# Optimization experiments

Measured on AMD Instinct MI355X. Metric: run time of the kernel, lower is better.

## Reference

```python
import jax, jax.numpy as jnp
import numpy as np
import math

B, T, D = 8, 1024, 1024
N, L = 256, 768
H = 16
TE = 2048  # time_embed_dim
EPS = 1e-5


def _ln(x, g, b):
    mu = jnp.mean(x, axis=-1, keepdims=True)
    var = jnp.mean(jnp.square(x - mu), axis=-1, keepdims=True)
    return (x - mu) * jax.lax.rsqrt(var + EPS) * g + b


def setup_inputs() -> dict:
    key = jax.random.key(0)
    ks = jax.random.split(key, 16)
    s = lambda fan_in: 1.0 / math.sqrt(fan_in)
    return {
        "x": jax.random.normal(ks[0], (B, T, D), jnp.float32),
        "xf": jax.random.normal(ks[1], (B, N, L), jnp.float32),
        "emb": jax.random.normal(ks[2], (B, TE), jnp.float32),
        "ln_g": jnp.ones((D,), jnp.float32),
        "ln_b": jnp.zeros((D,), jnp.float32),
        "cln_g": jnp.ones((L,), jnp.float32),
        "cln_b": jnp.zeros((L,), jnp.float32),
        "Wq": jax.random.normal(ks[3], (D, D), jnp.float32) * s(D),
        "bq": jnp.zeros((D,), jnp.float32),
        "Wk": jax.random.normal(ks[4], (L, D), jnp.float32) * s(L),
        "bk": jnp.zeros((D,), jnp.float32),
        "Wv": jax.random.normal(ks[5], (L, D), jnp.float32) * s(L),
        "bv": jnp.zeros((D,), jnp.float32),
        "sln_g": jnp.ones((D,), jnp.float32),
        "sln_b": jnp.zeros((D,), jnp.float32),
        "Wemb": jax.random.normal(ks[6], (TE, 2 * D), jnp.float32) * s(TE),
        "bemb": jnp.zeros((2 * D,), jnp.float32),
        "Wout": jax.random.normal(ks[7], (D, D), jnp.float32) * s(D) * 0.02,
        "bout": jnp.zeros((D,), jnp.float32),
    }


def reference(x, xf, emb, ln_g, ln_b, cln_g, cln_b, Wq, bq, Wk, bk, Wv, bv,
              sln_g, sln_b, Wemb, bemb, Wout, bout):
    # x: (B,T,D), xf: (B,N,L), emb: (B,TE)
    hd = D // H
    q = (_ln(x, ln_g, ln_b) @ Wq + bq).reshape(B, T, H, hd)
    xf_n = _ln(xf, cln_g, cln_b)
    k = (xf_n @ Wk + bk).reshape(B, N, H, hd)
    v = (xf_n @ Wv + bv).reshape(B, N, H, hd)
    # scores: (B,T,N,H); note: scaled by sqrt(D//H)
    att = jnp.einsum('bthd,bnhd->btnh', q, k) / math.sqrt(hd)
    w = jax.nn.softmax(att, axis=2)  # softmax over conditioning tokens N
    y = jnp.einsum('btnh,bnhd->bthd', w, v).reshape(B, T, D)
    # StylizationBlock (dropout = 0)
    emb_out = jax.nn.silu(emb) @ Wemb + bemb  # (B, 2D)
    scale, shift = jnp.split(emb_out[:, None, :], 2, axis=2)
    h = _ln(y, sln_g, sln_b) * (1.0 + scale) + shift
    h = jax.nn.silu(h) @ Wout + bout
    return x + h
```

## Files before the change

kernel.cpp:

```cpp
#include <hip/hip_runtime.h>
#include <hip/hip_bf16.h>

typedef __hip_bfloat16 bf16;
typedef unsigned short ushort;
typedef __attribute__((ext_vector_type(8))) short bf16x8;
typedef __attribute__((ext_vector_type(4))) float f32x4;

#define B_ 8
#define T_ 1024
#define D_ 1024
#define N_ 256
#define L_ 768
#define H_ 16
#define HD_ 64
#define TE_ 2048

__device__ __forceinline__ void gld16(const void* g, void* l) {
    __builtin_amdgcn_global_load_lds((const __attribute__((address_space(1))) void*)g,
                                     (__attribute__((address_space(3))) void*)l,
                                     16, 0, 0);
}

__device__ __forceinline__ float bitf(unsigned u) { return __uint_as_float(u); }

__global__ __launch_bounds__(256) void ln_both_kernel(const float* __restrict__ x,
                                                      const float* __restrict__ xf,
                                                      const float* __restrict__ g1,
                                                      const float* __restrict__ b1,
                                                      const float* __restrict__ g2,
                                                      const float* __restrict__ b2,
                                                      bf16* __restrict__ out1,
                                                      bf16* __restrict__ out2) {
    int row = blockIdx.x;
    int tid = threadIdx.x;
    const float *rp, *g, *bb; bf16* op; int cols;
    if (row < B_ * T_) {
        rp = x + (size_t)row * D_; g = g1; bb = b1; op = out1 + (size_t)row * D_; cols = D_;
    } else {
        int r = row - B_ * T_;
        rp = xf + (size_t)r * L_; g = g2; bb = b2; op = out2 + (size_t)r * L_; cols = L_;
    }
    bool act = tid * 4 < cols;
    float4 v = act ? *(const float4*)&rp[tid * 4] : make_float4(0.f, 0.f, 0.f, 0.f);
    float s = v.x + v.y + v.z + v.w;
    float s2 = v.x * v.x + v.y * v.y + v.z * v.z + v.w * v.w;
    for (int off = 32; off; off >>= 1) {
        s  += __shfl_down(s,  off, 64);
        s2 += __shfl_down(s2, off, 64);
    }
    __shared__ float ps[4], ps2[4];
    __shared__ float smu, srstd;
    int wid = tid >> 6, lid = tid & 63;
    if (lid == 0) { ps[wid] = s; ps2[wid] = s2; }
    __syncthreads();
    if (tid == 0) {
        float t = ps[0] + ps[1] + ps[2] + ps[3];
        float t2 = ps2[0] + ps2[1] + ps2[2] + ps2[3];
        float m = t / cols;
        float var = t2 / cols - m * m;
        smu = m; srstd = rsqrtf(var + 1e-5f);
    }
    __syncthreads();
    if (!act) return;
    float mu = smu, rstd = srstd;
    float4 gv = *(const float4*)&g[tid * 4];
    float4 bv = *(const float4*)&bb[tid * 4];
    float o0 = (v.x - mu) * rstd * gv.x + bv.x;
    float o1 = (v.y - mu) * rstd * gv.y + bv.y;
    float o2 = (v.z - mu) * rstd * gv.z + bv.z;
    float o3 = (v.w - mu) * rstd * gv.w + bv.w;
    ushort4 uo;
    bf16 h0 = __float2bfloat16(o0); uo.x = *(ushort*)&h0;
    bf16 h1 = __float2bfloat16(o1); uo.y = *(ushort*)&h1;
    bf16 h2 = __float2bfloat16(o2); uo.z = *(ushort*)&h2;
    bf16 h3 = __float2bfloat16(o3); uo.w = *(ushort*)&h3;
    *(ushort4*)&op[tid * 4] = uo;
}

__global__ __launch_bounds__(256) void tcvt4_kernel(const float* __restrict__ Wq,
                                                    const float* __restrict__ Wk,
                                                    const float* __restrict__ Wv,
                                                    const float* __restrict__ Wo,
                                                    bf16* __restrict__ wqt,
                                                    bf16* __restrict__ wkt,
                                                    bf16* __restrict__ wvt,
                                                    bf16* __restrict__ wot) {
    __shared__ ushort t[64][65];
    int y = blockIdx.y;
    const float* W; bf16* Wt; int K, ky;
    if (y < 16)      { W = Wq; Wt = wqt; K = 1024; ky = y; }
    else if (y < 28) { W = Wk; Wt = wkt; K = 768;  ky = y - 16; }
    else if (y < 40) { W = Wv; Wt = wvt; K = 768;  ky = y - 28; }
    else             { W = Wo; Wt = wot; K = 1024; ky = y - 40; }
    int k0 = ky * 64, n0 = blockIdx.x * 64;
    int tid = threadIdx.x;
#pragma unroll
    for (int i = 0; i < 16; i++) {
        int e = tid + i * 256;
        int r = e >> 6, c = e & 63;
        bf16 hv = __float2bfloat16(W[(size_t)(k0 + r) * D_ + n0 + c]);
        t[r][c] = *(ushort*)&hv;
    }
    __syncthreads();
#pragma unroll
    for (int i = 0; i < 16; i++) {
        int e = tid + i * 256;
        int r = e >> 6, c = e & 63;
        ushort uv = t[c][r];
        Wt[(size_t)(n0 + r) * K + k0 + c] = *(bf16*)&uv;
    }
}

template <int MODE>
__device__ __forceinline__ void gemm_body(const ushort* __restrict__ Ap,
                                          const ushort* __restrict__ Bp,
                                          const float* __restrict__ bias,
                                          const float* __restrict__ res,
                                          void* __restrict__ Cout,
                                          int m0, int n0, int Ncols, int K,
                                          ushort* Ash, ushort* Bsh) {
    int tid = threadIdx.x;
    int w = tid >> 6, lane = tid & 63;
    int quad = lane >> 4, l15 = lane & 15;
    int wm = (w >> 1) * 64, wn = (w & 1) * 64;
    int lr8 = lane >> 3;
    int sc  = lane & 7;
    int gc  = sc ^ lr8;
    f32x4 acc[4][4] = {};
    for (int kt = 0; kt < K; kt += 64) {
#pragma unroll
        for (int j = 0; j < 4; j++) {
            int rbase = w * 32 + j * 8;
            gld16(&Ap[(size_t)(m0 + rbase + lr8) * K + kt + gc * 8], &Ash[rbase * 64]);
            gld16(&Bp[(size_t)(n0 + rbase + lr8) * K + kt + gc * 8], &Bsh[rbase * 64]);
        }
        __syncthreads();
#pragma unroll
        for (int kh = 0; kh < 2; kh++) {
            bf16x8 af[4], bfr[4];
#pragma unroll
            for (int mt = 0; mt < 4; mt++)
                af[mt] = *(bf16x8*)&Ash[(wm + mt * 16 + l15) * 64 + (((kh * 4 + quad) ^ (l15 & 7)) * 8)];
#pragma unroll
            for (int nt = 0; nt < 4; nt++)
                bfr[nt] = *(bf16x8*)&Bsh[(wn + nt * 16 + l15) * 64 + (((kh * 4 + quad) ^ (l15 & 7)) * 8)];
#pragma unroll
            for (int mt = 0; mt < 4; mt++)
#pragma unroll
                for (int nt = 0; nt < 4; nt++)
                    acc[mt][nt] = __builtin_amdgcn_mfma_f32_16x16x32_bf16(af[mt], bfr[nt], acc[mt][nt], 0, 0, 0);
        }
        __syncthreads();
    }
#pragma unroll
    for (int mt = 0; mt < 4; mt++) {
#pragma unroll
        for (int nt = 0; nt < 4; nt++) {
#pragma unroll
            for (int reg = 0; reg < 4; reg++) {
                int row = m0 + wm + mt * 16 + quad * 4 + reg;
                int col = n0 + wn + nt * 16 + l15;
                float v = acc[mt][nt][reg] + bias[col];
                if (MODE == 1) {
                    v += res[(size_t)row * Ncols + col];
                    ((float*)Cout)[(size_t)row * Ncols + col] = v;
                } else if (MODE == 0) {
                    ((bf16*)Cout)[(size_t)row * Ncols + col] = __float2bfloat16(v);
                } else {
                    int b = row >> 8, n = row & 255;
                    int h = col >> 6, d = col & 63;
                    size_t addr = ((size_t)(b * 16 + h) * 64 + d) * 256
                                + (((n >> 3) ^ (d & 7)) * 8) + (n & 7);
                    ((bf16*)Cout)[addr] = __float2bfloat16(v);
                }
            }
        }
    }
}

__global__ __launch_bounds__(256) void qkv_gemm(const bf16* __restrict__ xn,
                                                const bf16* __restrict__ xfn,
                                                const bf16* __restrict__ wqt,
                                                const bf16* __restrict__ wkt,
                                                const bf16* __restrict__ wvt,
                                                const float* __restrict__ bq,
                                                const float* __restrict__ bk,
                                                const float* __restrict__ bv,
                                                bf16* __restrict__ q,
                                                bf16* __restrict__ kbuf,
                                                bf16* __restrict__ vT) {
    __shared__ ushort Ash[128 * 64];
    __shared__ ushort Bsh[128 * 64];
    int bid = blockIdx.x;
    if (bid < 512) {
        gemm_body<0>((const ushort*)xn, (const ushort*)wqt, bq, nullptr, q,
                     (bid & 63) * 128, (bid >> 6) * 128, D_, D_, Ash, Bsh);
    } else if (bid < 640) {
        int id = bid - 512;
        gemm_body<0>((const ushort*)xfn, (const ushort*)wkt, bk, nullptr, kbuf,
                     (id & 15) * 128, (id >> 4) * 128, D_, L_, Ash, Bsh);
    } else {
        int id = bid - 640;
        gemm_body<2>((const ushort*)xfn, (const ushort*)wvt, bv, nullptr, vT,
                     (id & 15) * 128, (id >> 4) * 128, D_, L_, Ash, Bsh);
    }
}

__global__ __launch_bounds__(256) void out_gemm(const bf16* __restrict__ a,
                                                const bf16* __restrict__ wot,
                                                const float* __restrict__ bout,
                                                const float* __restrict__ x,
                                                float* __restrict__ out) {
    __shared__ ushort Ash[128 * 64];
    __shared__ ushort Bsh[128 * 64];
    int bid = blockIdx.x;
    gemm_body<1>((const ushort*)a, (const ushort*)wot, bout, x, out,
                 (bid & 63) * 128, (bid >> 6) * 128, D_, D_, Ash, Bsh);
}

__global__ __launch_bounds__(256) void emb1_kernel(const float* __restrict__ emb,
                                                   const float* __restrict__ Wemb,
                                                   float* __restrict__ part) {
    __shared__ float se[8 * 256];
    __shared__ float red[16 * 8 * 64];
    int tid = threadIdx.x;
    int j0 = blockIdx.x * 64;
    int ks = blockIdx.y;
    int tx = tid & 15, ty = tid >> 4;
#pragma unroll
    for (int b = 0; b < 8; b++) {
        float xv = emb[b * TE_ + ks * 256 + tid];
        se[b * 256 + tid] = xv / (1.f + __expf(-xv));
    }
    __syncthreads();
    float acc[8][4] = {};
#pragma unroll 4
    for (int i = 0; i < 16; i++) {
        int e = ty + 16 * i;
        float4 wv = *(const float4*)&Wemb[(size_t)(ks * 256 + e) * 2048 + j0 + tx * 4];
#pragma unroll
        for (int b = 0; b < 8; b++) {
            float s = se[b * 256 + e];
            acc[b][0] += s * wv.x; acc[b][1] += s * wv.y;
            acc[b][2] += s * wv.z; acc[b][3] += s * wv.w;
        }
    }
#pragma unroll
    for (int b = 0; b < 8; b++)
#pragma unroll
        for (int m = 0; m < 4; m++)
            red[(ty * 8 + b) * 64 + tx * 4 + m] = acc[b][m];
    __syncthreads();
    for (int o = tid; o < 512; o += 256) {
        int b = o >> 6, jl = o & 63;
        float s = 0.f;
#pragma unroll
        for (int t2 = 0; t2 < 16; t2++) s += red[(t2 * 8 + b) * 64 + jl];
        part[((size_t)ks * 8 + b) * 2048 + j0 + jl] = s;
    }
}

__global__ __launch_bounds__(256) void emb2_kernel(const float* __restrict__ part,
                                                   const float* __restrict__ bemb,
                                                   float* __restrict__ embo) {
    int o = blockIdx.x * 256 + threadIdx.x;
    int b = o >> 11, j = o & 2047;
    float s = bemb[j];
#pragma unroll
    for (int ks = 0; ks < 8; ks++) s += part[((size_t)ks * 8 + b) * 2048 + j];
    embo[o] = s;
}

__global__ __launch_bounds__(256) void attn_mfma(const bf16* __restrict__ q,
                                                 const bf16* __restrict__ k,
                                                 const bf16* __restrict__ vT,
                                                 bf16* __restrict__ y) {
    __shared__ ushort KV[N_ * HD_];
    __shared__ ushort P[64 * N_];
    int tid = threadIdx.x;
    int w = tid >> 6, lane = tid & 63;
    int quad = lane >> 4, l15 = lane & 15;
    int t0 = blockIdx.x * 64;
    int bh = blockIdx.y;
    int b = bh >> 4, h = bh & 15;

    const ushort* kp = (const ushort*)k;
    const ushort* qp = (const ushort*)q;
    const ushort* vp = (const ushort*)vT;
    int lr8 = lane >> 3, sc = lane & 7, gc = sc ^ lr8;

#pragma unroll
    for (int j = 0; j < 8; j++) {
        int rbase = w * 64 + j * 8;
        gld16(&kp[(size_t)(b * N_ + rbase + lr8) * D_ + h * 64 + gc * 8], &KV[rbase * 64]);
    }
#pragma unroll
    for (int j = 0; j < 2; j++) {
        int rbase = w * 16 + j * 8;
        gld16(&qp[(size_t)(b * T_ + t0 + rbase + lr8) * D_ + h * 64 + gc * 8], &P[rbase * 64]);
    }
    __syncthreads();

    int qrow = w * 16 + l15;
    bf16x8 aq[2];
#pragma unroll
    for (int kk = 0; kk < 2; kk++)
        aq[kk] = *(bf16x8*)&P[qrow * 64 + (((kk * 4 + quad) ^ (qrow & 7)) * 8)];
    f32x4 sf[16];
#pragma unroll
    for (int nt = 0; nt < 16; nt++) {
        int n = nt * 16 + l15;
        bf16x8 b0 = *(bf16x8*)&KV[n * 64 + (((0 + quad) ^ (n & 7)) * 8)];
        bf16x8 b1 = *(bf16x8*)&KV[n * 64 + (((4 + quad) ^ (n & 7)) * 8)];
        f32x4 z = {};
        f32x4 t = __builtin_amdgcn_mfma_f32_16x16x32_bf16(aq[0], b0, z, 0, 0, 0);
        sf[nt] = __builtin_amdgcn_mfma_f32_16x16x32_bf16(aq[1], b1, t, 0, 0, 0);
    }
    __syncthreads();

    const ushort* vbase = vp + (size_t)(b * 16 + h) * 16384;
#pragma unroll
    for (int j = 0; j < 8; j++) {
        gld16(&vbase[(w * 8 + j) * 512 + lane * 8], &KV[(w * 8 + j) * 512]);
    }

    const float scale = 0.125f;
    float mx[4] = {-1e30f, -1e30f, -1e30f, -1e30f};
#pragma unroll
    for (int nt = 0; nt < 16; nt++)
#pragma unroll
        for (int reg = 0; reg < 4; reg++) mx[reg] = fmaxf(mx[reg], sf[nt][reg]);
#pragma unroll
    for (int off = 1; off < 16; off <<= 1)
#pragma unroll
        for (int reg = 0; reg < 4; reg++)
            mx[reg] = fmaxf(mx[reg], __shfl_xor(mx[reg], off, 64));
    float sm[4] = {0.f, 0.f, 0.f, 0.f};
#pragma unroll
    for (int nt = 0; nt < 16; nt++)
#pragma unroll
        for (int reg = 0; reg < 4; reg++) {
            float e = __expf((sf[nt][reg] - mx[reg]) * scale);
            sf[nt][reg] = e;
            sm[reg] += e;
        }
#pragma unroll
    for (int off = 1; off < 16; off <<= 1)
#pragma unroll
        for (int reg = 0; reg < 4; reg++)
            sm[reg] += __shfl_xor(sm[reg], off, 64);
    float inv[4];
#pragma unroll
    for (int reg = 0; reg < 4; reg++) inv[reg] = 1.f / sm[reg];

#pragma unroll
    for (int nt = 0; nt < 16; nt++)
#pragma unroll
        for (int reg = 0; reg < 4; reg++) {
            int r = w * 16 + quad * 4 + reg;
            int colc = nt * 2 + (l15 >> 3);
            int addr = r * 256 + ((colc ^ (r & 7)) * 8) + (l15 & 7);
            bf16 hv = __float2bfloat16(sf[nt][reg]);
            P[addr] = *(ushort*)&hv;
        }
    __syncthreads();

    f32x4 of[4] = {};
    int prow = w * 16 + l15;
#pragma unroll
    for (int kk = 0; kk < 8; kk++) {
        bf16x8 ap = *(bf16x8*)&P[prow * 256 + (((kk * 4 + quad) ^ (prow & 7)) * 8)];
#pragma unroll
        for (int dt = 0; dt < 4; dt++) {
            int d = dt * 16 + l15;
            bf16x8 bv = *(bf16x8*)&KV[d * 256 + (((kk * 4 + quad) ^ (d & 7)) * 8)];
            of[dt] = __builtin_amdgcn_mfma_f32_16x16x32_bf16(ap, bv, of[dt], 0, 0, 0);
        }
    }
#pragma unroll
    for (int dt = 0; dt < 4; dt++)
#pragma unroll
        for (int reg = 0; reg < 4; reg++) {
            int r = t0 + w * 16 + quad * 4 + reg;
            y[((size_t)(b * T_ + r) * D_) + h * 64 + dt * 16 + l15] =
                __float2bfloat16(of[dt][reg] * inv[reg]);
        }
}

__global__ __launch_bounds__(256) void styl_kernel(const bf16* __restrict__ y,
                                                   const float* __restrict__ g,
                                                   const float* __restrict__ bb,
                                                   const float* __restrict__ embo,
                                                   bf16* __restrict__ a) {
    int row = blockIdx.x;
    int b = row >> 10;
    int tid = threadIdx.x;
    const ushort* rp = (const ushort*)(y + (size_t)row * D_);
    ushort4 uy = *(const ushort4*)&rp[tid * 4];
    float v0 = bitf((unsigned)uy.x << 16), v1 = bitf((unsigned)uy.y << 16);
    float v2 = bitf((unsigned)uy.z << 16), v3 = bitf((unsigned)uy.w << 16);
    float s = v0 + v1 + v2 + v3;
    float s2 = v0 * v0 + v1 * v1 + v2 * v2 + v3 * v3;
    for (int off = 32; off; off >>= 1) {
        s  += __shfl_down(s,  off, 64);
        s2 += __shfl_down(s2, off, 64);
    }
    __shared__ float ps[4], ps2[4];
    __shared__ float smu, srstd;
    int wid = tid >> 6, lid = tid & 63;
    if (lid == 0) { ps[wid] = s; ps2[wid] = s2; }
    __syncthreads();
    if (tid == 0) {
        float t = ps[0] + ps[1] + ps[2] + ps[3];
        float t2 = ps2[0] + ps2[1] + ps2[2] + ps2[3];
        float m = t / D_;
        float var = t2 / D_ - m * m;
        smu = m; srstd = rsqrtf(var + 1e-5f);
    }
    __syncthreads();
    float mu = smu, rstd = srstd;
    float4 gv = *(const float4*)&g[tid * 4];
    float4 bv = *(const float4*)&bb[tid * 4];
    float4 scv = *(const float4*)&embo[b * 2048 + tid * 4];
    float4 shv = *(const float4*)&embo[b * 2048 + 1024 + tid * 4];
    float n0 = (v0 - mu) * rstd * gv.x + bv.x;
    float n1 = (v1 - mu) * rstd * gv.y + bv.y;
    float n2 = (v2 - mu) * rstd * gv.z + bv.z;
    float n3 = (v3 - mu) * rstd * gv.w + bv.w;
    float h0 = n0 * (1.f + scv.x) + shv.x;
    float h1 = n1 * (1.f + scv.y) + shv.y;
    float h2 = n2 * (1.f + scv.z) + shv.z;
    float h3 = n3 * (1.f + scv.w) + shv.w;
    h0 = h0 / (1.f + __expf(-h0));
    h1 = h1 / (1.f + __expf(-h1));
    h2 = h2 / (1.f + __expf(-h2));
    h3 = h3 / (1.f + __expf(-h3));
    ushort4 uo;
    bf16 t0 = __float2bfloat16(h0); uo.x = *(ushort*)&t0;
    bf16 t1 = __float2bfloat16(h1); uo.y = *(ushort*)&t1;
    bf16 t2 = __float2bfloat16(h2); uo.z = *(ushort*)&t2;
    bf16 t3 = __float2bfloat16(h3); uo.w = *(ushort*)&t3;
    *(ushort4*)&((ushort*)a)[(size_t)row * D_ + tid * 4] = uo;
}

extern "C" void kernel_launch(void* const* d_in, const int* in_sizes, int n_in,
                              void* d_out, int out_size, void* d_ws, size_t ws_size,
                              hipStream_t stream) {
    const float* x    = (const float*)d_in[0];
    const float* xf   = (const float*)d_in[1];
    const float* emb  = (const float*)d_in[2];
    const float* ln_g = (const float*)d_in[3];
    const float* ln_b = (const float*)d_in[4];
    const float* cln_g= (const float*)d_in[5];
    const float* cln_b= (const float*)d_in[6];
    const float* Wq   = (const float*)d_in[7];
    const float* bq   = (const float*)d_in[8];
    const float* Wk   = (const float*)d_in[9];
    const float* bk   = (const float*)d_in[10];
    const float* Wv   = (const float*)d_in[11];
    const float* bv   = (const float*)d_in[12];
    const float* sln_g= (const float*)d_in[13];
    const float* sln_b= (const float*)d_in[14];
    const float* Wemb = (const float*)d_in[15];
    const float* bemb = (const float*)d_in[16];
    const float* Wout = (const float*)d_in[17];
    const float* bout = (const float*)d_in[18];
    float* out = (float*)d_out;

    char* wsp = (char*)d_ws;
    bf16*  xn   = (bf16*)(wsp);
    bf16*  xfn  = (bf16*)(wsp + 16777216);
    bf16*  q    = (bf16*)(wsp + 19922944);
    bf16*  kbuf = (bf16*)(wsp + 36700160);
    bf16*  vT   = (bf16*)(wsp + 40894464);
    float* embo = (float*)(wsp + 45088768);
    bf16*  wqt  = (bf16*)(wsp + 45154304);
    bf16*  wkt  = (bf16*)(wsp + 47251456);
    bf16*  wvt  = (bf16*)(wsp + 48824320);
    bf16*  wot  = (bf16*)(wsp + 50397184);
    float* part = (float*)(wsp + 52494336);
    bf16*  ybuf = xn;
    bf16*  abuf = q;

    ln_both_kernel<<<B_ * T_ + B_ * N_, 256, 0, stream>>>(x, xf, ln_g, ln_b, cln_g, cln_b, xn, xfn);

    tcvt4_kernel<<<dim3(16, 56), 256, 0, stream>>>(Wq, Wk, Wv, Wout, wqt, wkt, wvt, wot);

    emb1_kernel<<<dim3(32, 8), 256, 0, stream>>>(emb, Wemb, part);
    emb2_kernel<<<64, 256, 0, stream>>>(part, bemb, embo);

    qkv_gemm<<<768, 256, 0, stream>>>(xn, xfn, wqt, wkt, wvt, bq, bk, bv, q, kbuf, vT);

    attn_mfma<<<dim3(16, 128), 256, 0, stream>>>(q, kbuf, vT, ybuf);

    styl_kernel<<<B_ * T_, 256, 0, stream>>>(ybuf, sln_g, sln_b, embo, abuf);

    out_gemm<<<512, 256, 0, stream>>>(abuf, wot, bout, x, out);
}
```

Before: 258.5 us.

## Merge prep kernels into one launch and shrink GEMM N-tile to 64

Folds the layernorm, weight transpose-convert and embedding partial-GEMV kernels into a single prep_kernel that dispatches on block index. The embedding reduction combine is moved into the QKV GEMM launch as extra blocks, and the embedding partial reduction now uses wave shuffles instead of a large shared buffer. The GEMM tile drops from 128x128 to 128x64 per block, doubling block count for better CU occupancy at the cost of less B-tile reuse and more A-tile reloads. Together these remove three kernel launches and the idle gaps between them.

```diff
diff --git a/kernel.cpp b/kernel.cpp
--- a/kernel.cpp
+++ b/kernel.cpp
@@ -23,91 +23,131 @@
 
 __device__ __forceinline__ float bitf(unsigned u) { return __uint_as_float(u); }
 
-__global__ __launch_bounds__(256) void ln_both_kernel(const float* __restrict__ x,
-                                                      const float* __restrict__ xf,
-                                                      const float* __restrict__ g1,
-                                                      const float* __restrict__ b1,
-                                                      const float* __restrict__ g2,
-                                                      const float* __restrict__ b2,
-                                                      bf16* __restrict__ out1,
-                                                      bf16* __restrict__ out2) {
-    int row = blockIdx.x;
+__global__ __launch_bounds__(256) void prep_kernel(
+        const float* __restrict__ x, const float* __restrict__ xf,
+        const float* __restrict__ g1, const float* __restrict__ b1,
+        const float* __restrict__ g2, const float* __restrict__ b2,
+        const float* __restrict__ Wq, const float* __restrict__ Wk,
+        const float* __restrict__ Wv, const float* __restrict__ Wo,
+        const float* __restrict__ emb, const float* __restrict__ Wemb,
+        bf16* __restrict__ out1, bf16* __restrict__ out2,
+        bf16* __restrict__ wqt, bf16* __restrict__ wkt,
+        bf16* __restrict__ wvt, bf16* __restrict__ wot,
+        float* __restrict__ part) {
+    __shared__ __align__(16) char smem[16384];
+    int bid = blockIdx.x;
     int tid = threadIdx.x;
-    const float *rp, *g, *bb; bf16* op; int cols;
-    if (row < B_ * T_) {
-        rp = x + (size_t)row * D_; g = g1; bb = b1; op = out1 + (size_t)row * D_; cols = D_;
+    if (bid < 10240) {
+        const float *rp, *g, *bb; bf16* op; int cols;
+        if (bid < B_ * T_) {
+            rp = x + (size_t)bid * D_; g = g1; bb = b1; op = out1 + (size_t)bid * D_; cols = D_;
+        } else {
+            int r = bid - B_ * T_;
+            rp = xf + (size_t)r * L_; g = g2; bb = b2; op = out2 + (size_t)r * L_; cols = L_;
+        }
+        float* ps  = (float*)smem;
+        float* ps2 = ps + 4;
+        float* st  = ps + 8;
+        bool act = tid * 4 < cols;
+        float4 v = act ? *(const float4*)&rp[tid * 4] : make_float4(0.f, 0.f, 0.f, 0.f);
+        float s = v.x + v.y + v.z + v.w;
+        float s2 = v.x * v.x + v.y * v.y + v.z * v.z + v.w * v.w;
+        for (int off = 32; off; off >>= 1) {
+            s  += __shfl_down(s,  off, 64);
+            s2 += __shfl_down(s2, off, 64);
+        }
+        int wid = tid >> 6, lid = tid & 63;
+        if (lid == 0) { ps[wid] = s; ps2[wid] = s2; }
+        __syncthreads();
+        if (tid == 0) {
+            float t = ps[0] + ps[1] + ps[2] + ps[3];
+            float t2 = ps2[0] + ps2[1] + ps2[2] + ps2[3];
+            float m = t / cols;
+            float var = t2 / cols - m * m;
+            st[0] = m; st[1] = rsqrtf(var + 1e-5f);
+        }
+        __syncthreads();
+        if (!act) return;
+        float mu = st[0], rstd = st[1];
+        float4 gv = *(const float4*)&g[tid * 4];
+        float4 bv = *(const float4*)&bb[tid * 4];
+        float o0 = (v.x - mu) * rstd * gv.x + bv.x;
+        float o1 = (v.y - mu) * rstd * gv.y + bv.y;
+        float o2 = (v.z - mu) * rstd * gv.z + bv.z;
+        float o3 = (v.w - mu) * rstd * gv.w + bv.w;
+        ushort4 uo;
+        bf16 h0 = __float2bfloat16(o0); uo.x = *(ushort*)&h0;
+        bf16 h1 = __float2bfloat16(o1); uo.y = *(ushort*)&h1;
+        bf16 h2 = __float2bfloat16(o2); uo.z = *(ushort*)&h2;
+        bf16 h3 = __float2bfloat16(o3); uo.w = *(ushort*)&h3;
+        *(ushort4*)&op[tid * 4] = uo;
+    } else if (bid < 11136) {
+        ushort (*t)[65] = (ushort(*)[65])smem;
+        int id = bid - 10240;
+        int xb = id & 15, y = id >> 4;
+        const float* W; bf16* Wt; int K, ky;
+        if (y < 16)      { W = Wq; Wt = wqt; K = 1024; ky = y; }
+        else if (y < 28) { W = Wk; Wt = wkt; K = 768;  ky = y - 16; }
+        else if (y < 40) { W = Wv; Wt = wvt; K = 768;  ky = y - 28; }
+        else             { W = Wo; Wt = wot; K = 1024; ky = y - 40; }
+        int k0 = ky * 64, n0 = xb * 64;
+#pragma unroll
+        for (int i = 0; i < 16; i++) {
+            int e = tid + i * 256;
+            int r = e >> 6, c = e & 63;
+            bf16 hv = __float2bfloat16(W[(size_t)(k0 + r) * D_ + n0 + c]);
+            t[r][c] = *(ushort*)&hv;
+        }
+        __syncthreads();
+#pragma unroll
+        for (int i = 0; i < 16; i++) {
+            int e = tid + i * 256;
+            int r = e >> 6, c = e & 63;
+            ushort uv = t[c][r];
+            Wt[(size_t)(n0 + r) * K + k0 + c] = *(bf16*)&uv;
+        }
     } else {
-        int r = row - B_ * T_;
-        rp = xf + (size_t)r * L_; g = g2; bb = b2; op = out2 + (size_t)r * L_; cols = L_;
-    }
-    bool act = tid * 4 < cols;
-    float4 v = act ? *(const float4*)&rp[tid * 4] : make_float4(0.f, 0.f, 0.f, 0.f);
-    float s = v.x + v.y + v.z + v.w;
-    float s2 = v.x * v.x + v.y * v.y + v.z * v.z + v.w * v.w;
-    for (int off = 32; off; off >>= 1) {
-        s  += __shfl_down(s,  off, 64);
-        s2 += __shfl_down(s2, off, 64);
-    }
-    __shared__ float ps[4], ps2[4];
-    __shared__ float smu, srstd;
-    int wid = tid >> 6, lid = tid & 63;
-    if (lid == 0) { ps[wid] = s; ps2[wid] = s2; }
-    __syncthreads();
-    if (tid == 0) {
-        float t = ps[0] + ps[1] + ps[2] + ps[3];
-        float t2 = ps2[0] + ps2[1] + ps2[2] + ps2[3];
-        float m = t / cols;
-        float var = t2 / cols - m * m;
-        smu = m; srstd = rsqrtf(var + 1e-5f);
-    }
-    __syncthreads();
-    if (!act) return;
-    float mu = smu, rstd = srstd;
-    float4 gv = *(const float4*)&g[tid * 4];
-    float4 bv = *(const float4*)&bb[tid * 4];
-    float o0 = (v.x - mu) * rstd * gv.x + bv.x;
-    float o1 = (v.y - mu) * rstd * gv.y + bv.y;
-    float o2 = (v.z - mu) * rstd * gv.z + bv.z;
-    float o3 = (v.w - mu) * rstd * gv.w + bv.w;
-    ushort4 uo;
-    bf16 h0 = __float2bfloat16(o0); uo.x = *(ushort*)&h0;
-    bf16 h1 = __float2bfloat16(o1); uo.y = *(ushort*)&h1;
-    bf16 h2 = __float2bfloat16(o2); uo.z = *(ushort*)&h2;
-    bf16 h3 = __float2bfloat16(o3); uo.w = *(ushort*)&h3;
-    *(ushort4*)&op[tid * 4] = uo;
-}
-
-__global__ __launch_bounds__(256) void tcvt4_kernel(const float* __restrict__ Wq,
-                                                    const float* __restrict__ Wk,
-                                                    const float* __restrict__ Wv,
-                                                    const float* __restrict__ Wo,
-                                                    bf16* __restrict__ wqt,
-                                                    bf16* __restrict__ wkt,
-                                                    bf16* __restrict__ wvt,
-                                                    bf16* __restrict__ wot) {
-    __shared__ ushort t[64][65];
-    int y = blockIdx.y;
-    const float* W; bf16* Wt; int K, ky;
-    if (y < 16)      { W = Wq; Wt = wqt; K = 1024; ky = y; }
-    else if (y < 28) { W = Wk; Wt = wkt; K = 768;  ky = y - 16; }
-    else if (y < 40) { W = Wv; Wt = wvt; K = 768;  ky = y - 28; }
-    else             { W = Wo; Wt = wot; K = 1024; ky = y - 40; }
-    int k0 = ky * 64, n0 = blockIdx.x * 64;
-    int tid = threadIdx.x;
-#pragma unroll
-    for (int i = 0; i < 16; i++) {
-        int e = tid + i * 256;
-        int r = e >> 6, c = e & 63;
-        bf16 hv = __float2bfloat16(W[(size_t)(k0 + r) * D_ + n0 + c]);
-        t[r][c] = *(ushort*)&hv;
-    }
-    __syncthreads();
-#pragma unroll
-    for (int i = 0; i < 16; i++) {
-        int e = tid + i * 256;
-        int r = e >> 6, c = e & 63;
-        ushort uv = t[c][r];
-        Wt[(size_t)(n0 + r) * K + k0 + c] = *(bf16*)&uv;
+        float* se  = (float*)smem;
+        float* red = (float*)(smem + 8192);
+        int id = bid - 11136;
+        int j0 = (id & 31) * 64;
+        int ks = id >> 5;
+        int tx = tid & 15, ty = tid >> 4;
+        int w = tid >> 6, lane = tid & 63;
+#pragma unroll
+        for (int b = 0; b < 8; b++) {
+            float xv = emb[b * TE_ + ks * 256 + tid];
+            se[b * 256 + tid] = xv / (1.f + __expf(-xv));
+        }
+        __syncthreads();
+        float acc[8][4] = {};
+#pragma unroll 4
+        for (int i = 0; i < 16; i++) {
+            int e = ty + 16 * i;
+            float4 wv = *(const float4*)&Wemb[(size_t)(ks * 256 + e) * 2048 + j0 + tx * 4];
+#pragma unroll
+            for (int b = 0; b < 8; b++) {
+                float s = se[b * 256 + e];
+                acc[b][0] += s * wv.x; acc[b][1] += s * wv.y;
+                acc[b][2] += s * wv.z; acc[b][3] += s * wv.w;
+            }
+        }
+#pragma unroll
+        for (int b = 0; b < 8; b++)
+#pragma unroll
+            for (int m = 0; m < 4; m++) {
+                float v = acc[b][m];
+                v += __shfl_down(v, 32, 64);
+                v += __shfl_down(v, 16, 64);
+                if (lane < 16) red[(w * 8 + b) * 64 + lane * 4 + m] = v;
+            }
+        __syncthreads();
+        for (int o = tid; o < 512; o += 256) {
+            int b = o >> 6, jl = o & 63;
+            float s = red[(0 * 8 + b) * 64 + jl] + red[(1 * 8 + b) * 64 + jl]
+                    + red[(2 * 8 + b) * 64 + jl] + red[(3 * 8 + b) * 64 + jl];
+            part[((size_t)ks * 8 + b) * 2048 + j0 + jl] = s;
+        }
     }
 }
 
@@ -122,32 +162,36 @@
     int tid = threadIdx.x;
     int w = tid >> 6, lane = tid & 63;
     int quad = lane >> 4, l15 = lane & 15;
-    int wm = (w >> 1) * 64, wn = (w & 1) * 64;
+    int wm = (w >> 1) * 64, wn = (w & 1) * 32;
     int lr8 = lane >> 3;
     int sc  = lane & 7;
     int gc  = sc ^ lr8;
-    f32x4 acc[4][4] = {};
+    f32x4 acc[4][2] = {};
     for (int kt = 0; kt < K; kt += 64) {
 #pragma unroll
         for (int j = 0; j < 4; j++) {
             int rbase = w * 32 + j * 8;
             gld16(&Ap[(size_t)(m0 + rbase + lr8) * K + kt + gc * 8], &Ash[rbase * 64]);
+        }
+#pragma unroll
+        for (int j = 0; j < 2; j++) {
+            int rbase = w * 16 + j * 8;
             gld16(&Bp[(size_t)(n0 + rbase + lr8) * K + kt + gc * 8], &Bsh[rbase * 64]);
         }
         __syncthreads();
 #pragma unroll
         for (int kh = 0; kh < 2; kh++) {
-            bf16x8 af[4], bfr[4];
+            bf16x8 af[4], bfr[2];
 #pragma unroll
             for (int mt = 0; mt < 4; mt++)
                 af[mt] = *(bf16x8*)&Ash[(wm + mt * 16 + l15) * 64 + (((kh * 4 + quad) ^ (l15 & 7)) * 8)];
 #pragma unroll
-            for (int nt = 0; nt < 4; nt++)
+            for (int nt = 0; nt < 2; nt++)
                 bfr[nt] = *(bf16x8*)&Bsh[(wn + nt * 16 + l15) * 64 + (((kh * 4 + quad) ^ (l15 & 7)) * 8)];
 #pragma unroll
             for (int mt = 0; mt < 4; mt++)
 #pragma unroll
-                for (int nt = 0; nt < 4; nt++)
+                for (int nt = 0; nt < 2; nt++)
                     acc[mt][nt] = __builtin_amdgcn_mfma_f32_16x16x32_bf16(af[mt], bfr[nt], acc[mt][nt], 0, 0, 0);
         }
         __syncthreads();
@@ -155,7 +199,7 @@
 #pragma unroll
     for (int mt = 0; mt < 4; mt++) {
 #pragma unroll
-        for (int nt = 0; nt < 4; nt++) {
+        for (int nt = 0; nt < 2; nt++) {
 #pragma unroll
             for (int reg = 0; reg < 4; reg++) {
                 int row = m0 + wm + mt * 16 + quad * 4 + reg;
@@ -188,21 +232,31 @@
                                                 const float* __restrict__ bv,
                                                 bf16* __restrict__ q,
                                                 bf16* __restrict__ kbuf,
-                                                bf16* __restrict__ vT) {
+                                                bf16* __restrict__ vT,
+                                                const float* __restrict__ part,
+                                                const float* __restrict__ bemb,
+                                                float* __restrict__ embo) {
     __shared__ ushort Ash[128 * 64];
-    __shared__ ushort Bsh[128 * 64];
+    __shared__ ushort Bsh[64 * 64];
     int bid = blockIdx.x;
-    if (bid < 512) {
+    if (bid < 1024) {
         gemm_body<0>((const ushort*)xn, (const ushort*)wqt, bq, nullptr, q,
-                     (bid & 63) * 128, (bid >> 6) * 128, D_, D_, Ash, Bsh);
-    } else if (bid < 640) {
-        int id = bid - 512;
+                     (bid & 63) * 128, (bid >> 6) * 64, D_, D_, Ash, Bsh);
+    } else if (bid < 1280) {
+        int id = bid - 1024;
         gemm_body<0>((const ushort*)xfn, (const ushort*)wkt, bk, nullptr, kbuf,
-                     (id & 15) * 128, (id >> 4) * 128, D_, L_, Ash, Bsh);
+                     (id & 15) * 128, (id >> 4) * 64, D_, L_, Ash, Bsh);
+    } else if (bid < 1536) {
+        int id = bid - 1280;
+        gemm_body<2>((const ushort*)xfn, (const ushort*)wvt, bv, nullptr, vT,
+                     (id & 15) * 128, (id >> 4) * 64, D_, L_, Ash, Bsh);
     } else {
-        int id = bid - 640;
-        gemm_body<2>((const ushort*)xfn, (const ushort*)wvt, bv, nullptr, vT,
-                     (id & 15) * 128, (id >> 4) * 128, D_, L_, Ash, Bsh);
+        int o = (bid - 1536) * 256 + threadIdx.x;
+        int b = o >> 11, j = o & 2047;
+        float s = bemb[j];
+#pragma unroll
+        for (int ks = 0; ks < 8; ks++) s += part[((size_t)ks * 8 + b) * 2048 + j];
+        embo[o] = s;
     }
 }
 
@@ -212,63 +266,10 @@
                                                 const float* __restrict__ x,
                                                 float* __restrict__ out) {
     __shared__ ushort Ash[128 * 64];
-    __shared__ ushort Bsh[128 * 64];
+    __shared__ ushort Bsh[64 * 64];
     int bid = blockIdx.x;
     gemm_body<1>((const ushort*)a, (const ushort*)wot, bout, x, out,
-                 (bid & 63) * 128, (bid >> 6) * 128, D_, D_, Ash, Bsh);
-}
-
-__global__ __launch_bounds__(256) void emb1_kernel(const float* __restrict__ emb,
-                                                   const float* __restrict__ Wemb,
-                                                   float* __restrict__ part) {
-    __shared__ float se[8 * 256];
-    __shared__ float red[16 * 8 * 64];
-    int tid = threadIdx.x;
-    int j0 = blockIdx.x * 64;
-    int ks = blockIdx.y;
-    int tx = tid & 15, ty = tid >> 4;
-#pragma unroll
-    for (int b = 0; b < 8; b++) {
-        float xv = emb[b * TE_ + ks * 256 + tid];
-        se[b * 256 + tid] = xv / (1.f + __expf(-xv));
-    }
-    __syncthreads();
-    float acc[8][4] = {};
-#pragma unroll 4
-    for (int i = 0; i < 16; i++) {
-        int e = ty + 16 * i;
-        float4 wv = *(const float4*)&Wemb[(size_t)(ks * 256 + e) * 2048 + j0 + tx * 4];
-#pragma unroll
-        for (int b = 0; b < 8; b++) {
-            float s = se[b * 256 + e];
-            acc[b][0] += s * wv.x; acc[b][1] += s * wv.y;
-            acc[b][2] += s * wv.z; acc[b][3] += s * wv.w;
-        }
-    }
-#pragma unroll
-    for (int b = 0; b < 8; b++)
-#pragma unroll
-        for (int m = 0; m < 4; m++)
-            red[(ty * 8 + b) * 64 + tx * 4 + m] = acc[b][m];
-    __syncthreads();
-    for (int o = tid; o < 512; o += 256) {
-        int b = o >> 6, jl = o & 63;
-        float s = 0.f;
-#pragma unroll
-        for (int t2 = 0; t2 < 16; t2++) s += red[(t2 * 8 + b) * 64 + jl];
-        part[((size_t)ks * 8 + b) * 2048 + j0 + jl] = s;
-    }
-}
-
-__global__ __launch_bounds__(256) void emb2_kernel(const float* __restrict__ part,
-                                                   const float* __restrict__ bemb,
-                                                   float* __restrict__ embo) {
-    int o = blockIdx.x * 256 + threadIdx.x;
-    int b = o >> 11, j = o & 2047;
-    float s = bemb[j];
-#pragma unroll
-    for (int ks = 0; ks < 8; ks++) s += part[((size_t)ks * 8 + b) * 2048 + j];
-    embo[o] = s;
+                 (bid & 63) * 128, (bid >> 6) * 64, D_, D_, Ash, Bsh);
 }
 
 __global__ __launch_bounds__(256) void attn_mfma(const bf16* __restrict__ q,
@@ -482,18 +483,16 @@
     bf16*  ybuf = xn;
     bf16*  abuf = q;
 
-    ln_both_kernel<<<B_ * T_ + B_ * N_, 256, 0, stream>>>(x, xf, ln_g, ln_b, cln_g, cln_b, xn, xfn);
-
-    tcvt4_kernel<<<dim3(16, 56), 256, 0, stream>>>(Wq, Wk, Wv, Wout, wqt, wkt, wvt, wot);
-
-    emb1_kernel<<<dim3(32, 8), 256, 0, stream>>>(emb, Wemb, part);
-    emb2_kernel<<<64, 256, 0, stream>>>(part, bemb, embo);
-
-    qkv_gemm<<<768, 256, 0, stream>>>(xn, xfn, wqt, wkt, wvt, bq, bk, bv, q, kbuf, vT);
+    prep_kernel<<<11392, 256, 0, stream>>>(x, xf, ln_g, ln_b, cln_g, cln_b,
+                                           Wq, Wk, Wv, Wout, emb, Wemb,
+                                           xn, xfn, wqt, wkt, wvt, wot, part);
+
+    qkv_gemm<<<1600, 256, 0, stream>>>(xn, xfn, wqt, wkt, wvt, bq, bk, bv,
+                                       q, kbuf, vT, part, bemb, embo);
 
     attn_mfma<<<dim3(16, 128), 256, 0, stream>>>(q, kbuf, vT, ybuf);
 
     styl_kernel<<<B_ * T_, 256, 0, stream>>>(ybuf, sln_g, sln_b, embo, abuf);
 
-    out_gemm<<<512, 256, 0, stream>>>(abuf, wot, bout, x, out);
-}
+    out_gemm<<<1024, 256, 0, stream>>>(abuf, wot, bout, x, out);
+}
```

Measured after the change: 255.8 us. About the same (-1.1%).
